# Kernel optimization log

Hardware: AMD Instinct MI355X
Metric: run time of the kernel (lower is better)

The kernel has to match this reference:

```python
import jax, jax.numpy as jnp
import numpy as np

# ---- config (mirrors cfg / init kwargs) ----
FEAT_STRIDE = 16
IM_DIMS = (1024, 1024)          # (height, width)
ANCHOR_SCALES = (8, 16, 32)
ANCHOR_RATIOS = (0.5, 1.0, 2.0)
PRE_NMS_TOPN = 6000             # eval mode (cfg_key=1)
POST_NMS_TOPN = 300
NMS_THRESH = 0.7
MIN_SIZE = 16


def _generate_base_anchors(base_size=16, ratios=ANCHOR_RATIOS, scales=ANCHOR_SCALES):
    """py-faster-rcnn generate_anchors, in numpy (static)."""
    def mk(ws, hs, xc, yc):
        return np.stack([xc - 0.5 * (ws - 1), yc - 0.5 * (hs - 1),
                         xc + 0.5 * (ws - 1), yc + 0.5 * (hs - 1)], axis=1)
    base = np.array([0, 0, base_size - 1, base_size - 1], dtype=np.float64)
    w = base[2] - base[0] + 1; h = base[3] - base[1] + 1
    xc = base[0] + 0.5 * (w - 1); yc = base[1] + 0.5 * (h - 1)
    # ratio enum
    size = w * h
    ws = np.round(np.sqrt(size / np.array(ratios)))
    hs = np.round(ws * np.array(ratios))
    ratio_anchors = mk(ws, hs, xc, yc)
    # scale enum
    out = []
    for a in ratio_anchors:
        aw = a[2] - a[0] + 1; ah = a[3] - a[1] + 1
        axc = a[0] + 0.5 * (aw - 1); ayc = a[1] + 0.5 * (ah - 1)
        out.append(mk(aw * np.array(scales), ah * np.array(scales), axc, ayc))
    return np.concatenate(out, axis=0).astype(np.float32)  # [A,4]


def _all_anchors(H, W):
    base = _generate_base_anchors()                       # [A,4]
    sx = np.arange(W) * FEAT_STRIDE
    sy = np.arange(H) * FEAT_STRIDE
    sx, sy = np.meshgrid(sx, sy)
    shifts = np.stack([sx.ravel(), sy.ravel(), sx.ravel(), sy.ravel()], axis=1)  # [H*W,4]
    anchors = shifts[:, None, :].astype(np.float32) + base[None, :, :]
    return anchors.reshape(-1, 4)                         # [H*W*A, 4]


def setup_inputs() -> dict:
    key = jax.random.key(0)
    k1, k2 = jax.random.split(key)
    H, W, A = 64, 64, 9
    rpn_cls_score = jax.random.normal(k1, (1, H, W, 2 * A), dtype=jnp.float32)
    rpn_bbox_pred = jax.random.normal(k2, (1, H, W, 4 * A), dtype=jnp.float32)
    return {"rpn_cls_score": rpn_cls_score, "rpn_bbox_pred": rpn_bbox_pred}


def _proposals(rpn_cls_score, rpn_bbox_pred):
    _, H, W, C2 = rpn_cls_score.shape
    A = C2 // 2
    # rpn_softmax: per-anchor 2-way softmax, foreground prob
    scores = jax.nn.softmax(rpn_cls_score.reshape(H, W, A, 2), axis=-1)[..., 1].reshape(-1)  # [N]
    deltas = rpn_bbox_pred.reshape(-1, 4)                  # [N,4]
    anchors = jnp.asarray(_all_anchors(H, W))              # [N,4]
    # bbox_transform_inv
    aw = anchors[:, 2] - anchors[:, 0] + 1.0
    ah = anchors[:, 3] - anchors[:, 1] + 1.0
    axc = anchors[:, 0] + 0.5 * aw
    ayc = anchors[:, 1] + 0.5 * ah
    dx, dy, dw, dh = deltas[:, 0], deltas[:, 1], deltas[:, 2], deltas[:, 3]
    pxc = dx * aw + axc; pyc = dy * ah + ayc
    pw = jnp.exp(dw) * aw; ph = jnp.exp(dh) * ah
    x1 = pxc - 0.5 * pw; y1 = pyc - 0.5 * ph
    x2 = pxc + 0.5 * pw; y2 = pyc + 0.5 * ph
    # clip to image
    im_h, im_w = IM_DIMS
    x1 = jnp.clip(x1, 0.0, im_w - 1.0); x2 = jnp.clip(x2, 0.0, im_w - 1.0)
    y1 = jnp.clip(y1, 0.0, im_h - 1.0); y2 = jnp.clip(y2, 0.0, im_h - 1.0)
    boxes = jnp.stack([x1, y1, x2, y2], axis=1)            # [N,4]
    # filter too-small boxes by masking their score
    valid = ((x2 - x1 + 1.0) >= MIN_SIZE) & ((y2 - y1 + 1.0) >= MIN_SIZE)
    scores = jnp.where(valid, scores, -jnp.inf)
    return boxes, scores


def _nms_keep(boxes, K):
    """Greedy NMS keep-mask over score-descending boxes [K,4]."""
    x1, y1, x2, y2 = boxes[:, 0], boxes[:, 1], boxes[:, 2], boxes[:, 3]
    areas = (x2 - x1 + 1.0) * (y2 - y1 + 1.0)
    ix1 = jnp.maximum(x1[:, None], x1[None, :])
    iy1 = jnp.maximum(y1[:, None], y1[None, :])
    ix2 = jnp.minimum(x2[:, None], x2[None, :])
    iy2 = jnp.minimum(y2[:, None], y2[None, :])
    iw = jnp.maximum(ix2 - ix1 + 1.0, 0.0)
    ih = jnp.maximum(iy2 - iy1 + 1.0, 0.0)
    inter = iw * ih
    iou = inter / (areas[:, None] + areas[None, :] - inter)  # [K,K]
    idxs = jnp.arange(K)
    def body(i, keep):
        sup = keep[i] & (iou[i] > NMS_THRESH) & (idxs > i)
        return keep & ~sup
    return jax.lax.fori_loop(0, K, body, jnp.ones((K,), bool))


def reference(rpn_cls_score, rpn_bbox_pred):
    boxes, scores = _proposals(rpn_cls_score, rpn_bbox_pred)
    K = min(PRE_NMS_TOPN, scores.shape[0])
    top_scores, order = jax.lax.top_k(scores, K)           # score-descending
    top_boxes = boxes[order]                               # [K,4]
    keep = _nms_keep(top_boxes, K)
    sel_scores = jnp.where(keep, top_scores, -jnp.inf)
    _, idx = jax.lax.top_k(sel_scores, POST_NMS_TOPN)      # kept, in score order
    out_boxes = top_boxes[idx]                             # [post,4]
    blob = jnp.concatenate([jnp.zeros((POST_NMS_TOPN, 1), out_boxes.dtype), out_boxes], axis=1)
    return blob                                            # [post,5] (batch_idx, x1,y1,x2,y2)
```

## Files before the change

### kernel.cpp

```cpp
#include <hip/hip_runtime.h>
#include <stdint.h>

typedef unsigned long long u64;
typedef unsigned int u32;

#define N_ANCH 36864
#define WGRID 64
#define A_PER 9
#define KTOP 6000
#define NOUT 300
#define NBIN 5120
#define NCHK 94
#define NCH2 47
#define NJ   6016
#define INF_BIN 0
#define SLOTS 4
#define SPILLCAP 32

#define BARRIER_LDS() do {                                   \
    asm volatile("s_waitcnt lgkmcnt(0)" ::: "memory");       \
    __builtin_amdgcn_s_barrier();                            \
    asm volatile("" ::: "memory");                           \
} while (0)

__constant__ float c_ax1[9] = {-84.f,-176.f,-360.f,-56.f,-120.f,-248.f,-36.f,-80.f,-168.f};
__constant__ float c_ay1[9] = {-40.f,-88.f,-184.f,-56.f,-120.f,-248.f,-80.f,-168.f,-344.f};
__constant__ float c_aw[9]  = {184.f,368.f,736.f,128.f,256.f,512.f,88.f,176.f,352.f};
__constant__ float c_ah[9]  = {96.f,192.f,384.f,128.f,256.f,512.f,176.f,352.f,704.f};

__device__ __forceinline__ u32 binof(u32 u) {
    if (u < 0x80000000u) return 0u;
    if (u < 0xBF000000u) return 1u + ((u - 0x80000000u) >> 22);
    return 256u + ((u - 0xBF000000u) >> 11);
}

__global__ __launch_bounds__(256) void proposal_kernel(const float* __restrict__ cls,
                                                       const float* __restrict__ dlt,
                                                       u64* __restrict__ keys,
                                                       float4* __restrict__ boxes,
                                                       u32* __restrict__ hist) {
    __shared__ u32 lh[NBIN];
    const int t = threadIdx.x;
    for (int b = t; b < NBIN; b += 256) lh[b] = 0;
    __syncthreads();

    int i = blockIdx.x * 256 + t;
    int a  = i % A_PER;
    int hw = i / A_PER;
    int wx = hw % WGRID;
    int hy = hw / WGRID;

    float2 lp = *(const float2*)(cls + hw * 18 + 2 * a);
    float l0 = lp.x, l1 = lp.y;
    float m  = fmaxf(l0, l1);
    float e0 = expf(l0 - m), e1 = expf(l1 - m);
    float s  = e1 / (e0 + e1);

    float4 dd = *(const float4*)(dlt + hw * 36 + 4 * a);
    float dx = dd.x, dy = dd.y, dw = dd.z, dh = dd.w;
    float aw = c_aw[a], ah = c_ah[a];
    float axc = (c_ax1[a] + 16.f * (float)wx) + 0.5f * aw;
    float ayc = (c_ay1[a] + 16.f * (float)hy) + 0.5f * ah;

    float pxc = dx * aw + axc;
    float pyc = dy * ah + ayc;
    float pw  = expf(dw) * aw;
    float ph  = expf(dh) * ah;
    float x1 = pxc - 0.5f * pw, y1 = pyc - 0.5f * ph;
    float x2 = pxc + 0.5f * pw, y2 = pyc + 0.5f * ph;
    x1 = fminf(fmaxf(x1, 0.f), 1023.f);
    x2 = fminf(fmaxf(x2, 0.f), 1023.f);
    y1 = fminf(fmaxf(y1, 0.f), 1023.f);
    y2 = fminf(fmaxf(y2, 0.f), 1023.f);
    bool valid = ((x2 - x1 + 1.f) >= 16.f) && ((y2 - y1 + 1.f) >= 16.f);
    float sc = valid ? s : -__builtin_huge_valf();

    u32 sb  = __float_as_uint(sc);
    u32 ord = (sb & 0x80000000u) ? ~sb : (sb | 0x80000000u);
    u64 key = ((u64)ord << 32) | (u32)(~(u32)i);
    keys[i]  = key;
    boxes[i] = make_float4(x1, y1, x2, y2);

    u64 infb = __ballot(!valid);
    if (valid) {
        atomicAdd(&lh[binof(ord)], 1u);
    } else {
        int lane = t & 63;
        if (lane == __builtin_ctzll(infb))
            atomicAdd(&lh[INF_BIN], (u32)__popcll(infb));
    }
    __syncthreads();
    for (int b = t; b < NBIN; b += 256) {
        u32 v = lh[b];
        if (v) atomicAdd(&hist[b], v);
    }
}

__global__ __launch_bounds__(1024) void scan_kernel(const u32* __restrict__ hist,
                                                    u32* __restrict__ binStart,
                                                    u32* __restrict__ gEV) {
    __shared__ u32 wsum[16];
    const int t = threadIdx.x;
    const int lane = t & 63;
    const int v = t >> 6;
    if (t == 0) gEV[1] = KTOP;
    int hi = NBIN - 1 - 5 * t;
    u32 cnt[5];
    u32 sum = 0;
#pragma unroll
    for (int k = 0; k < 5; ++k) { cnt[k] = hist[hi - k]; sum += cnt[k]; }
    u32 s = sum;
#pragma unroll
    for (int d = 1; d < 64; d <<= 1) {
        u32 x = __shfl_up(s, d, 64);
        if (lane >= d) s += x;
    }
    if (lane == 63) wsum[v] = s;
    __syncthreads();
    u32 base = 0;
#pragma unroll
    for (int q = 0; q < 16; ++q) {
        u32 x = wsum[q];
        if (q < v) base += x;
    }
    u32 run = base + s - sum;
#pragma unroll
    for (int k = 0; k < 5; ++k) {
        int b = hi - k;
        binStart[b] = run;
        u32 end = run + cnt[k];
        if (run < KTOP && end >= KTOP) gEV[0] = end;
        run = end;
    }
}

__global__ void scatter_kernel(const u64* __restrict__ keys,
                               const u32* __restrict__ binStart,
                               u32* __restrict__ cursor,
                               u64* __restrict__ scat) {
    int i = blockIdx.x * blockDim.x + threadIdx.x;
    if (i >= N_ANCH) return;
    u64 k = keys[i];
    u32 b = binof((u32)(k >> 32));
    u32 s = binStart[b];
    if (s < KTOP) {
        u32 p = s + atomicAdd(&cursor[b], 1u);
        scat[p] = k;
    }
}

__global__ void rank_kernel(const u64* __restrict__ scat,
                            const u32* __restrict__ binStart,
                            const u32* __restrict__ hist,
                            const float4* __restrict__ boxes,
                            const u32* __restrict__ gEV,
                            float4* __restrict__ topBoxes,
                            int* __restrict__ gV) {
    int i = blockIdx.x * blockDim.x + threadIdx.x;
    u32 E = gEV[0];
    if (i >= (int)E) return;
    u64 k = scat[i];
    u32 b = binof((u32)(k >> 32));
    u32 s = binStart[b], c = hist[b];
    u32 r = s;
    for (u32 j = s; j < s + c; ++j) r += (scat[j] > k) ? 1u : 0u;
    if (r < KTOP) {
        int idx = (int)(~(u32)k);
        topBoxes[r] = boxes[idx];
        if (!(k >> 63)) atomicMin(gV, (int)r);
    }
}

__device__ __forceinline__ bool iou_gt(float4 a, float areaA, float4 b, float areaB) {
    float ix1 = fmaxf(a.x, b.x), iy1 = fmaxf(a.y, b.y);
    float ix2 = fminf(a.z, b.z), iy2 = fminf(a.w, b.w);
    float iw = fmaxf(ix2 - ix1 + 1.0f, 0.0f);
    float ih = fmaxf(iy2 - iy1 + 1.0f, 0.0f);
    float inter = iw * ih;
    float iou = inter / (areaA + areaB - inter);
    return iou > 0.7f;
}

__global__ __launch_bounds__(256) void maskT_kernel(const float4* __restrict__ topBoxes,
                                                    const u32* __restrict__ gEV,
                                                    u64* __restrict__ S) {
    const int V = (int)gEV[1];
    const int nch = (V + 63) >> 6;
    const int jc = blockIdx.x;
    const int w0 = blockIdx.y * 4;
    if (jc >= nch || w0 > jc) return;
    __shared__ float4 cb[256];
    __shared__ float  ca[256];
    const int t = threadIdx.x;
    const int lane = t & 63;
    {
        int ci = w0 * 64 + t;
        float4 b = (ci < V) ? topBoxes[ci] : make_float4(0.f, 0.f, -8.f, -8.f);
        cb[t] = b;
        ca[t] = (b.z - b.x + 1.f) * (b.w - b.y + 1.f);
    }
    __syncthreads();
    const int w = w0 + (t >> 6);
    if (w > jc || w >= nch) return;
    const int j = jc * 64 + lane;
    float4 bj = (j < V) ? topBoxes[j] : make_float4(0.f, 0.f, -8.f, -8.f);
    float aj = (bj.z - bj.x + 1.f) * (bj.w - bj.y + 1.f);
    const int s0 = (t >> 6) * 64;
    u64 m = 0;
#pragma unroll 4
    for (int b = 0; b < 64; ++b)
        if (iou_gt(bj, aj, cb[s0 + b], ca[s0 + b])) m |= (1ull << b);
    if (w == jc) m &= ((1ull << lane) - 1ull);
    S[(u64)w * NJ + j] = m;
}

__global__ __launch_bounds__(1024) void nms_out_kernel(const float4* __restrict__ topBoxes,
                                                       const u32* __restrict__ gEV,
                                                       const u64* __restrict__ S,
                                                       float* __restrict__ out) {
    __shared__ u64 dA[NCH2][64];
    __shared__ u64 dAB[NCH2][64];
    __shared__ u64 dB[NCH2][64];
    __shared__ u64 keepw[NCHK];
    __shared__ u64 supw[2][32];
    __shared__ u64 spillK[SPILLCAP];
    __shared__ u32 spillW[SPILLCAP];
    __shared__ u32 wsum[16];
    const int t = threadIdx.x;
    const int lane = t & 63;
    const int v = t >> 6;
    const int V = (int)gEV[1];
    const int nch = (V + 63) >> 6;
    const int nr  = (nch + 1) >> 1;
    if (t < NCHK) keepw[t] = 0;
    for (int idx = t; idx < nr * 64; idx += 1024) {
        int r = idx >> 6, l = idx & 63;
        dA[r][l]  = S[(u64)(2 * r) * NJ + 128 * r + l];
        dAB[r][l] = S[(u64)(2 * r) * NJ + 128 * r + 64 + l];
        dB[r][l]  = S[(u64)(2 * r + 1) * NJ + 128 * r + 64 + l];
    }
    __syncthreads();

    u64 kwS[SLOTS], pA[SLOTS], pB[SLOTS], aofs[SLOTS];
#pragma unroll
    for (int k = 0; k < SLOTS; ++k) { kwS[k] = 0; pA[k] = 0; pB[k] = 0; aofs[k] = 0; }
    int nslot = 0, nspill = 0, nkept = 0;

    for (int r = 0; r < nr; ++r) {
        const int par = r & 1;
        u64 accA = 0, accB = 0;
#pragma unroll
        for (int k = 0; k < SLOTS; ++k) {
            if (nslot > 16 * k + v) { accA |= pA[k] & kwS[k]; accB |= pB[k] & kwS[k]; }
        }
        for (int s = 0; s < nspill; ++s) {
            u64 kk = spillK[s];
            const u64* row = S + (u64)spillW[s] * NJ + 128 * r + lane;
            accA |= row[0] & kk; accB |= row[64] & kk;
        }
        u64 bA = __ballot(accA != 0ull), bB = __ballot(accB != 0ull);
        if (lane == 0) { supw[par][v] = bA; supw[par][16 + v] = bB; }
        if (r + 1 < nr) {
            u64 ofsn = (u64)(128 * (r + 1)) + lane;
#pragma unroll
            for (int k = 0; k < SLOTS; ++k)
                if (nslot > 16 * k + v) { pA[k] = S[aofs[k] + ofsn]; pB[k] = S[aofs[k] + ofsn + 64]; }
        }
        BARRIER_LDS();
        u64 x = supw[par][lane & 31];
#pragma unroll
        for (int m = 1; m < 16; m <<= 1) x |= __shfl_xor(x, m, 64);
        u64 rwA = __shfl(x, 0, 64);
        u64 rwB = __shfl(x, 16, 64);
        int remA = V - 128 * r;
        int remB = remA - 64;
        u64 aliveA = (remA >= 64) ? ~0ull : ((remA <= 0) ? 0ull : ((1ull << remA) - 1ull));
        u64 aliveB = (remB >= 64) ? ~0ull : ((remB <= 0) ? 0ull : ((1ull << remB) - 1ull));
        u64 dAl = dA[r][lane], dABl = dAB[r][lane], dBl = dB[r][lane];
        u64 candA = ~rwA & aliveA, kbA = 0;
        while (candA) {
            int b = __builtin_ctzll(candA);
            kbA |= (1ull << b);
            candA &= ~(1ull << b);
            candA &= ~__ballot(((dAl >> b) & 1ull) != 0ull);
        }
        u64 supAB = __ballot((dABl & kbA) != 0ull);
        u64 candB = ~(rwB | supAB) & aliveB, kbB = 0;
        while (candB) {
            int b = __builtin_ctzll(candB);
            kbB |= (1ull << b);
            candB &= ~(1ull << b);
            candB &= ~__ballot(((dBl >> b) & 1ull) != 0ull);
        }
        if (t == 0) { keepw[2 * r] = kbA; if (2 * r + 1 < nch) keepw[2 * r + 1] = kbB; }
        bool sadd = false;
        if (kbA) {
            int so = nslot & 15, si = nslot >> 4;
            if (si < SLOTS) {
                if (v == so) {
#pragma unroll
                    for (int k = 0; k < SLOTS; ++k) if (k == si) {
                        kwS[k] = kbA; aofs[k] = (u64)(2 * r) * NJ;
                        if (r + 1 < nr) {
                            u64 o = (u64)(128 * (r + 1)) + lane;
                            pA[k] = S[aofs[k] + o]; pB[k] = S[aofs[k] + o + 64];
                        }
                    }
                }
                ++nslot;
            } else if (nspill < SPILLCAP) {
                if (v == 15 && lane == 0) { spillW[nspill] = 2 * r; spillK[nspill] = kbA; }
                ++nspill; sadd = true;
            }
        }
        if (kbB) {
            int so = nslot & 15, si = nslot >> 4;
            if (si < SLOTS) {
                if (v == so) {
#pragma unroll
                    for (int k = 0; k < SLOTS; ++k) if (k == si) {
                        kwS[k] = kbB; aofs[k] = (u64)(2 * r + 1) * NJ;
                        if (r + 1 < nr) {
                            u64 o = (u64)(128 * (r + 1)) + lane;
                            pA[k] = S[aofs[k] + o]; pB[k] = S[aofs[k] + o + 64];
                        }
                    }
                }
                ++nslot;
            } else if (nspill < SPILLCAP) {
                if (v == 15 && lane == 0) { spillW[nspill] = 2 * r + 1; spillK[nspill] = kbB; }
                ++nspill; sadd = true;
            }
        }
        if (sadd) BARRIER_LDS();
        nkept += __popcll(kbA) + __popcll(kbB);
        if (nkept >= NOUT) break;
    }
    __syncthreads();

    const int per = 6;
    int r0 = t * per;
    int r1 = min(r0 + per, KTOP);
    u32 cnt = 0;
    for (int r = r0; r < r1; ++r)
        cnt += (u32)((keepw[r >> 6] >> (r & 63)) & 1ull);
    u32 s = cnt;
#pragma unroll
    for (int d = 1; d < 64; d <<= 1) {
        u32 x = __shfl_up(s, d, 64);
        if (lane >= d) s += x;
    }
    if (lane == 63) wsum[v] = s;
    __syncthreads();
    u32 base = 0;
    u32 total = 0;
#pragma unroll
    for (int q = 0; q < 16; ++q) {
        u32 x = wsum[q];
        if (q < v) base += x;
        total += x;
    }
    const int n1 = min((int)total, NOUT);
    int kp = (int)(base + s - cnt);
    for (int r = r0; r < r1; ++r) {
        int kept = (int)((keepw[r >> 6] >> (r & 63)) & 1ull);
        int pos = kept ? kp : (n1 + r - kp);
        if (pos < NOUT) {
            float4 b = topBoxes[r];
            out[pos * 5 + 0] = 0.f;
            out[pos * 5 + 1] = b.x;
            out[pos * 5 + 2] = b.y;
            out[pos * 5 + 3] = b.z;
            out[pos * 5 + 4] = b.w;
        }
        kp += kept;
    }
}

extern "C" void kernel_launch(void* const* d_in, const int* in_sizes, int n_in,
                              void* d_out, int out_size, void* d_ws, size_t ws_size,
                              hipStream_t stream) {
    const float* cls = (const float*)d_in[0];
    const float* dlt = (const float*)d_in[1];
    float* out = (float*)d_out;
    char* ws = (char*)d_ws;
    u64*    keys     = (u64*)   (ws);
    u64*    scat     = (u64*)   (ws + 294912);
    float4* boxes    = (float4*)(ws + 589824);
    float4* topBoxes = (float4*)(ws + 1179648);
    u32*    hist     = (u32*)   (ws + 1275648);
    u32*    cursor   = (u32*)   (ws + 1296128);
    u32*    binStart = (u32*)   (ws + 1316608);
    u32*    gEV      = (u32*)   (ws + 1337088);
    u64*    S        = (u64*)   (ws + 1337344);

    hipMemsetAsync(hist, 0, 2 * NBIN * sizeof(u32), stream);
    proposal_kernel<<<144, 256, 0, stream>>>(cls, dlt, keys, boxes, hist);
    scan_kernel<<<1, 1024, 0, stream>>>(hist, binStart, gEV);
    scatter_kernel<<<(N_ANCH + 255) / 256, 256, 0, stream>>>(keys, binStart, cursor, scat);
    rank_kernel<<<(N_ANCH + 255) / 256, 256, 0, stream>>>(scat, binStart, hist, boxes, gEV,
                                                          topBoxes, (int*)&gEV[1]);
    maskT_kernel<<<dim3(NCHK, (NCHK + 3) / 4), 256, 0, stream>>>(topBoxes, gEV, S);
    nms_out_kernel<<<1, 1024, 0, stream>>>(topBoxes, gEV, S, out);
}
```

Measured before the change: 130.2 us.

## Shrink serial NMS block to four wavefronts with more register slots

The single-block NMS kernel drops from 16 wavefronts to 4. Each wave now holds up to 10 kept-row register slots instead of 4, and spilled rows are split across waves. The per-row cross-wave reduction becomes a direct OR of 8 shared words instead of a shuffle tree, which is meant to make the per-iteration barrier and reduction cheaper. In exchange there are fewer parallel loads, more registers per thread, and the output compaction does 24 elements per thread instead of 6.

```diff
diff --git a/kernel.cpp b/kernel.cpp
--- a/kernel.cpp
+++ b/kernel.cpp
@@ -14,8 +14,9 @@
 #define NCH2 47
 #define NJ   6016
 #define INF_BIN 0
-#define SLOTS 4
-#define SPILLCAP 32
+#define NMSW 4
+#define SLOTS 10
+#define SPILLCAP 64
 
 #define BARRIER_LDS() do {                                   \
     asm volatile("s_waitcnt lgkmcnt(0)" ::: "memory");       \
@@ -214,18 +215,18 @@
     S[(u64)w * NJ + j] = m;
 }
 
-__global__ __launch_bounds__(1024) void nms_out_kernel(const float4* __restrict__ topBoxes,
-                                                       const u32* __restrict__ gEV,
-                                                       const u64* __restrict__ S,
-                                                       float* __restrict__ out) {
+__global__ __launch_bounds__(256) void nms_out_kernel(const float4* __restrict__ topBoxes,
+                                                      const u32* __restrict__ gEV,
+                                                      const u64* __restrict__ S,
+                                                      float* __restrict__ out) {
     __shared__ u64 dA[NCH2][64];
     __shared__ u64 dAB[NCH2][64];
     __shared__ u64 dB[NCH2][64];
     __shared__ u64 keepw[NCHK];
-    __shared__ u64 supw[2][32];
+    __shared__ u64 supw[2][2 * NMSW];
     __shared__ u64 spillK[SPILLCAP];
     __shared__ u32 spillW[SPILLCAP];
-    __shared__ u32 wsum[16];
+    __shared__ u32 wsum[NMSW];
     const int t = threadIdx.x;
     const int lane = t & 63;
     const int v = t >> 6;
@@ -233,7 +234,7 @@
     const int nch = (V + 63) >> 6;
     const int nr  = (nch + 1) >> 1;
     if (t < NCHK) keepw[t] = 0;
-    for (int idx = t; idx < nr * 64; idx += 1024) {
+    for (int idx = t; idx < nr * 64; idx += 256) {
         int r = idx >> 6, l = idx & 63;
         dA[r][l]  = S[(u64)(2 * r) * NJ + 128 * r + l];
         dAB[r][l] = S[(u64)(2 * r) * NJ + 128 * r + 64 + l];
@@ -251,27 +252,24 @@
         u64 accA = 0, accB = 0;
 #pragma unroll
         for (int k = 0; k < SLOTS; ++k) {
-            if (nslot > 16 * k + v) { accA |= pA[k] & kwS[k]; accB |= pB[k] & kwS[k]; }
-        }
-        for (int s = 0; s < nspill; ++s) {
+            if (nslot > NMSW * k + v) { accA |= pA[k] & kwS[k]; accB |= pB[k] & kwS[k]; }
+        }
+        for (int s = v; s < nspill; s += NMSW) {
             u64 kk = spillK[s];
             const u64* row = S + (u64)spillW[s] * NJ + 128 * r + lane;
             accA |= row[0] & kk; accB |= row[64] & kk;
         }
         u64 bA = __ballot(accA != 0ull), bB = __ballot(accB != 0ull);
-        if (lane == 0) { supw[par][v] = bA; supw[par][16 + v] = bB; }
+        if (lane == 0) { supw[par][v] = bA; supw[par][NMSW + v] = bB; }
         if (r + 1 < nr) {
             u64 ofsn = (u64)(128 * (r + 1)) + lane;
 #pragma unroll
             for (int k = 0; k < SLOTS; ++k)
-                if (nslot > 16 * k + v) { pA[k] = S[aofs[k] + ofsn]; pB[k] = S[aofs[k] + ofsn + 64]; }
+                if (nslot > NMSW * k + v) { pA[k] = S[aofs[k] + ofsn]; pB[k] = S[aofs[k] + ofsn + 64]; }
         }
         BARRIER_LDS();
-        u64 x = supw[par][lane & 31];
-#pragma unroll
-        for (int m = 1; m < 16; m <<= 1) x |= __shfl_xor(x, m, 64);
-        u64 rwA = __shfl(x, 0, 64);
-        u64 rwB = __shfl(x, 16, 64);
+        u64 rwA = supw[par][0] | supw[par][1] | supw[par][2] | supw[par][3];
+        u64 rwB = supw[par][4] | supw[par][5] | supw[par][6] | supw[par][7];
         int remA = V - 128 * r;
         int remB = remA - 64;
         u64 aliveA = (remA >= 64) ? ~0ull : ((remA <= 0) ? 0ull : ((1ull << remA) - 1ull));
@@ -295,7 +293,7 @@
         if (t == 0) { keepw[2 * r] = kbA; if (2 * r + 1 < nch) keepw[2 * r + 1] = kbB; }
         bool sadd = false;
         if (kbA) {
-            int so = nslot & 15, si = nslot >> 4;
+            int so = nslot & (NMSW - 1), si = nslot >> 2;
             if (si < SLOTS) {
                 if (v == so) {
 #pragma unroll
@@ -309,12 +307,12 @@
                 }
                 ++nslot;
             } else if (nspill < SPILLCAP) {
-                if (v == 15 && lane == 0) { spillW[nspill] = 2 * r; spillK[nspill] = kbA; }
+                if (v == NMSW - 1 && lane == 0) { spillW[nspill] = 2 * r; spillK[nspill] = kbA; }
                 ++nspill; sadd = true;
             }
         }
         if (kbB) {
-            int so = nslot & 15, si = nslot >> 4;
+            int so = nslot & (NMSW - 1), si = nslot >> 2;
             if (si < SLOTS) {
                 if (v == so) {
 #pragma unroll
@@ -328,7 +326,7 @@
                 }
                 ++nslot;
             } else if (nspill < SPILLCAP) {
-                if (v == 15 && lane == 0) { spillW[nspill] = 2 * r + 1; spillK[nspill] = kbB; }
+                if (v == NMSW - 1 && lane == 0) { spillW[nspill] = 2 * r + 1; spillK[nspill] = kbB; }
                 ++nspill; sadd = true;
             }
         }
@@ -338,7 +336,7 @@
     }
     __syncthreads();
 
-    const int per = 6;
+    const int per = 24;
     int r0 = t * per;
     int r1 = min(r0 + per, KTOP);
     u32 cnt = 0;
@@ -355,7 +353,7 @@
     u32 base = 0;
     u32 total = 0;
 #pragma unroll
-    for (int q = 0; q < 16; ++q) {
+    for (int q = 0; q < NMSW; ++q) {
         u32 x = wsum[q];
         if (q < v) base += x;
         total += x;
@@ -401,5 +399,5 @@
     rank_kernel<<<(N_ANCH + 255) / 256, 256, 0, stream>>>(scat, binStart, hist, boxes, gEV,
                                                           topBoxes, (int*)&gEV[1]);
     maskT_kernel<<<dim3(NCHK, (NCHK + 3) / 4), 256, 0, stream>>>(topBoxes, gEV, S);
-    nms_out_kernel<<<1, 1024, 0, stream>>>(topBoxes, gEV, S, out);
-}
+    nms_out_kernel<<<1, 256, 0, stream>>>(topBoxes, gEV, S, out);
+}
```

Result: faster. 120.7 us (-7.3%).
